# Kernel tuning notes

Measured on AMD Instinct MI355X. Metric: run time of the kernel, lower is better.

The kernel has to match this reference:

```python
import jax, jax.numpy as jnp
import numpy as np

NEG_INF = -1e30


def setup_inputs() -> dict:
    key = jax.random.key(0)
    ks = jax.random.split(key, 5)
    B, S, D, H = 2, 2048, 1024, 16
    sc = 0.02  # weight init scale
    return {
        "x": jax.random.normal(ks[0], (B, S, D), dtype=jnp.float32),
        "Wq": jax.random.normal(ks[1], (D, D), dtype=jnp.float32) * sc,
        "bq": jnp.zeros((D,), dtype=jnp.float32),
        "Wk": jax.random.normal(ks[2], (D, D), dtype=jnp.float32) * sc,
        "bk": jnp.zeros((D,), dtype=jnp.float32),
        "Wv": jax.random.normal(ks[3], (D, D), dtype=jnp.float32) * sc,
        "bv": jnp.zeros((D,), dtype=jnp.float32),
        "Wo": jax.random.normal(ks[4], (D, D), dtype=jnp.float32) * sc,
        "bo": jnp.zeros((D,), dtype=jnp.float32),
        "temperature": jnp.ones((H,), dtype=jnp.float32),
    }


def reference(x, Wq, bq, Wk, bk, Wv, bv, Wo, bo, temperature):
    B, S, D = x.shape
    H = temperature.shape[0]
    hd = D // H
    sparsity = 0.8
    k = max(1, int(S * (1.0 - sparsity)))
    scale = hd ** (-0.5)

    # torch Linear: y = x @ W^T + b ; reshape to [B, S, H, hd] -> [B, H, S, hd]
    def proj(W, b):
        return (x @ W.T + b).reshape(B, S, H, hd).transpose(0, 2, 1, 3)

    q, kk, v = proj(Wq, bq), proj(Wk, bk), proj(Wv, bv)

    temp = jnp.clip(temperature, 0.1, None)[None, :, None, None]  # [1,H,1,1]
    scores = jnp.einsum("bhqd,bhkd->bhqk", q, kk) * scale / temp  # [B,H,S,S]

    # top-k sparsity: keep the k largest scores per row, -inf elsewhere.
    # Equivalent to torch's topk+scatter for distinct values: threshold at
    # the k-th largest value per row.
    topk_vals = jax.lax.top_k(scores, k)[0]           # [B,H,S,k]
    kth = topk_vals[..., -1:]                          # [B,H,S,1]
    sparse_scores = jnp.where(scores >= kth, scores, NEG_INF)

    attn = jax.nn.softmax(sparse_scores, axis=-1)      # [B,H,S,S]
    head_out = jnp.einsum("bhqk,bhkd->bhqd", attn, v)  # [B,H,S,hd]

    # stack heads back: [B,S,H,hd] -> [B,S,D], then out projection
    out = head_out.transpose(0, 2, 1, 3).reshape(B, S, D)
    out = out @ Wo.T + bo

    avg_attention = attn.mean(axis=1)                  # [B,S,S]
    return out, avg_attention
```

## Files before the change

kernel.cpp:

```cpp
#include <hip/hip_runtime.h>
#include <stdint.h>

#define S_LEN 2048
#define D_DIM 1024
#define NHEAD 16
#define HD    64
#define TOPK  409

typedef unsigned short u16;
typedef __attribute__((ext_vector_type(8))) short bf16x8;
typedef __attribute__((ext_vector_type(4))) float f32x4;
#define MFMA __builtin_amdgcn_mfma_f32_16x16x32_bf16

__device__ __forceinline__ u16 f2b(float f) {
    unsigned u = __float_as_uint(f);
    return (u16)((u + 0x7fffu + ((u >> 16) & 1u)) >> 16);
}
__device__ __forceinline__ float b2f(u16 h) {
    return __uint_as_float(((unsigned)h) << 16);
}

__global__ __launch_bounds__(256, 4)
void split_f32(const float* __restrict__ src, u16* __restrict__ hi,
               u16* __restrict__ lo, int n4)
{
    const int i = blockIdx.x * 256 + threadIdx.x;
    if (i >= n4) return;
    const float4 v = ((const float4*)src)[i];
    const float vv[4] = {v.x, v.y, v.z, v.w};
    u16 h4[4], l4[4];
#pragma unroll
    for (int c = 0; c < 4; ++c) {
        h4[c] = f2b(vv[c]);
        l4[c] = f2b(vv[c] - b2f(h4[c]));
    }
    ((ushort4*)hi)[i] = make_ushort4(h4[0], h4[1], h4[2], h4[3]);
    ((ushort4*)lo)[i] = make_ushort4(l4[0], l4[1], l4[2], l4[3]);
}

template<int MODE>
__global__ __launch_bounds__(512, 2)
void proj_mfma(const u16* __restrict__ Ahi, const u16* __restrict__ Alo,
               const u16* __restrict__ Whi, const u16* __restrict__ Wlo,
               const float* __restrict__ bias, float* __restrict__ outf,
               u16* __restrict__ o1, u16* __restrict__ o2)
{
    const int t = threadIdx.x, w = t >> 6, l = t & 63;
    const int lq = l & 15, quad = l >> 4;
    const int m0 = blockIdx.y * 128 + (w >> 2) * 64;
    const int n0 = blockIdx.x * 128 + (w & 3) * 32;

    f32x4 acc[4][2];
#pragma unroll
    for (int i = 0; i < 4; ++i)
#pragma unroll
        for (int j = 0; j < 2; ++j) acc[i][j] = (f32x4){0.f, 0.f, 0.f, 0.f};

    const size_t abase = (size_t)(m0 + lq) * D_DIM + quad * 8;
    const size_t bbase = (size_t)(n0 + lq) * D_DIM + quad * 8;

#pragma unroll 2
    for (int k0 = 0; k0 < D_DIM; k0 += 32) {
        bf16x8 ah[4], al[4], bh[2], bl[2];
#pragma unroll
        for (int i = 0; i < 4; ++i) {
            ah[i] = *(const bf16x8*)(Ahi + abase + (size_t)i * 16 * D_DIM + k0);
            al[i] = *(const bf16x8*)(Alo + abase + (size_t)i * 16 * D_DIM + k0);
        }
#pragma unroll
        for (int j = 0; j < 2; ++j) {
            bh[j] = *(const bf16x8*)(Whi + bbase + (size_t)j * 16 * D_DIM + k0);
            bl[j] = *(const bf16x8*)(Wlo + bbase + (size_t)j * 16 * D_DIM + k0);
        }
#pragma unroll
        for (int i = 0; i < 4; ++i)
#pragma unroll
            for (int j = 0; j < 2; ++j) {
                acc[i][j] = MFMA(ah[i], bh[j], acc[i][j], 0, 0, 0);
                acc[i][j] = MFMA(ah[i], bl[j], acc[i][j], 0, 0, 0);
                acc[i][j] = MFMA(al[i], bh[j], acc[i][j], 0, 0, 0);
            }
    }

#pragma unroll
    for (int j = 0; j < 2; ++j) {
        const int n = n0 + j * 16 + lq;
        const float bb = bias[n];
        const int hh = n >> 6, ee = n & 63;
#pragma unroll
        for (int i = 0; i < 4; ++i) {
            const int mb = m0 + i * 16 + quad * 4;
            const int bbm = mb >> 11, ss = mb & 2047;
            if (MODE == 2) {
#pragma unroll
                for (int r = 0; r < 4; ++r)
                    outf[(size_t)(mb + r) * D_DIM + n] = acc[i][j][r] + bb;
            } else if (MODE == 1) {
                ushort4 pk;
                pk.x = f2b(acc[i][j][0] + bb);
                pk.y = f2b(acc[i][j][1] + bb);
                pk.z = f2b(acc[i][j][2] + bb);
                pk.w = f2b(acc[i][j][3] + bb);
                *(ushort4*)(o1 + ((size_t)((bbm * NHEAD + hh) * HD + ee)) * S_LEN + ss) = pk;
            } else {
#pragma unroll
                for (int r = 0; r < 4; ++r) {
                    const float v = acc[i][j][r] + bb;
                    const size_t idx = ((size_t)(bbm * NHEAD + hh) * S_LEN + ss + r) * HD + ee;
                    const u16 h = f2b(v);
                    o1[idx] = h;
                    o2[idx] = f2b(v - b2f(h));
                }
            }
        }
    }
}

__global__ __launch_bounds__(512, 2)
void attn_mfma(const u16* __restrict__ Qhi, const u16* __restrict__ Qlo,
               const u16* __restrict__ Khi, const u16* __restrict__ Klo,
               const u16* __restrict__ Vt,  const float* __restrict__ temp,
               u16* __restrict__ HOhi, u16* __restrict__ HOlo,
               float* __restrict__ avg)
{
    __shared__ __align__(16) u16 aLds[16 * 2056];
    __shared__ float pvpart[4 * 16 * 16];
    __shared__ int   cnts[16][8][5];
    __shared__ float red[16][8][2];
    __shared__ float rowMu[16], rowSig[16], rowLo[16], rowHi[16], rowZi[16];

    const int t = threadIdx.x, w = t >> 6, l = t & 63;
    const int lq = l & 15, quad = l >> 4;
    const int b  = blockIdx.x >> 7;
    const int q0 = (blockIdx.x & 127) << 4;

    float avgreg[64];
#pragma unroll
    for (int i = 0; i < 64; ++i) avgreg[i] = 0.f;

#pragma unroll 1
    for (int h = 0; h < NHEAD; ++h) {
        const size_t bh = (size_t)(b * NHEAD + h) * S_LEN;
        const float tscale = 0.125f / fmaxf(temp[h], 0.1f);

        const u16* qph = Qhi + (bh + q0 + lq) * HD + quad * 8;
        const u16* qpl = Qlo + (bh + q0 + lq) * HD + quad * 8;
        const bf16x8 qh0 = *(const bf16x8*)qph;
        const bf16x8 qh1 = *(const bf16x8*)(qph + 32);
        const bf16x8 ql0 = *(const bf16x8*)qpl;
        const bf16x8 ql1 = *(const bf16x8*)(qpl + 32);

        f32x4 acc[16];
        const u16* kph = Khi + (bh + w * 256 + lq) * HD + quad * 8;
        const u16* kpl = Klo + (bh + w * 256 + lq) * HD + quad * 8;
#pragma unroll
        for (int tt = 0; tt < 16; ++tt) {
            const bf16x8 k0 = *(const bf16x8*)(kph + tt * 16 * HD);
            const bf16x8 k1 = *(const bf16x8*)(kph + tt * 16 * HD + 32);
            const bf16x8 m0 = *(const bf16x8*)(kpl + tt * 16 * HD);
            const bf16x8 m1 = *(const bf16x8*)(kpl + tt * 16 * HD + 32);
            f32x4 a = {0.f, 0.f, 0.f, 0.f};
            a = MFMA(qh0, k0, a, 0, 0, 0);
            a = MFMA(qh1, k1, a, 0, 0, 0);
            a = MFMA(qh0, m0, a, 0, 0, 0);
            a = MFMA(qh1, m1, a, 0, 0, 0);
            a = MFMA(ql0, k0, a, 0, 0, 0);
            a = MFMA(ql1, k1, a, 0, 0, 0);
            acc[tt] = a * tscale;
        }
        __syncthreads();

        {
            float s1[4] = {0.f,0.f,0.f,0.f}, s2[4] = {0.f,0.f,0.f,0.f};
#pragma unroll
            for (int tt = 0; tt < 16; ++tt)
#pragma unroll
                for (int r = 0; r < 4; ++r) {
                    const float v = acc[tt][r];
                    s1[r] += v;
                    s2[r] = __fmaf_rn(v, v, s2[r]);
                }
#pragma unroll
            for (int off = 1; off < 16; off <<= 1)
#pragma unroll
                for (int r = 0; r < 4; ++r) {
                    s1[r] += __shfl_xor(s1[r], off, 16);
                    s2[r] += __shfl_xor(s2[r], off, 16);
                }
            if (lq == 0)
#pragma unroll
                for (int r = 0; r < 4; ++r) {
                    red[quad * 4 + r][w][0] = s1[r];
                    red[quad * 4 + r][w][1] = s2[r];
                }
        }
        __syncthreads();
        if (t < 16) {
            float a = 0.f, c = 0.f;
#pragma unroll
            for (int ww = 0; ww < 8; ++ww) { a += red[t][ww][0]; c += red[t][ww][1]; }
            const float mu = a * (1.f / 2048.f);
            const float va = c * (1.f / 2048.f) - mu * mu;
            rowMu[t] = mu;
            rowSig[t] = sqrtf(fmaxf(va, 0.f));
        }
        __syncthreads();

        {
            float th[5][4];
            int c[5][4];
#pragma unroll
            for (int r = 0; r < 4; ++r) {
                const float mu = rowMu[quad * 4 + r], sg = rowSig[quad * 4 + r];
#pragma unroll
                for (int i = 0; i < 5; ++i) {
                    th[i][r] = __fmaf_rn(sg, 0.55f + 0.15f * (float)i, mu);
                    c[i][r] = 0;
                }
            }
#pragma unroll
            for (int tt = 0; tt < 16; ++tt)
#pragma unroll
                for (int r = 0; r < 4; ++r) {
                    const float v = acc[tt][r];
#pragma unroll
                    for (int i = 0; i < 5; ++i) c[i][r] += (v >= th[i][r]) ? 1 : 0;
                }
#pragma unroll
            for (int off = 1; off < 16; off <<= 1)
#pragma unroll
                for (int i = 0; i < 5; ++i)
#pragma unroll
                    for (int r = 0; r < 4; ++r) c[i][r] += __shfl_xor(c[i][r], off, 16);
            if (lq == 0)
#pragma unroll
                for (int r = 0; r < 4; ++r)
#pragma unroll
                    for (int i = 0; i < 5; ++i) cnts[quad * 4 + r][w][i] = c[i][r];
        }
        __syncthreads();
        if (t < 16) {
            int c[5] = {0, 0, 0, 0, 0};
#pragma unroll
            for (int ww = 0; ww < 8; ++ww)
#pragma unroll
                for (int i = 0; i < 5; ++i) c[i] += cnts[t][ww][i];
            const float mu = rowMu[t], sg = rowSig[t];
            float lo, hi;
            if (c[0] < TOPK) {
                lo = __fmaf_rn(sg, -6.f, mu);
                hi = __fmaf_rn(sg, 0.55f + 0.15f * 0.f, mu);
            } else if (c[4] >= TOPK) {
                lo = __fmaf_rn(sg, 0.55f + 0.15f * 4.f, mu);
                hi = __fmaf_rn(sg, 6.f, mu);
            } else {
                int bi = 0;
#pragma unroll
                for (int j = 1; j < 4; ++j) if (c[j] >= TOPK) bi = j;
                lo = __fmaf_rn(sg, 0.55f + 0.15f * (float)bi, mu);
                hi = __fmaf_rn(sg, 0.55f + 0.15f * (float)(bi + 1), mu);
            }
            rowLo[t] = lo;
            rowHi[t] = hi;
        }
        __syncthreads();

#pragma unroll 1
        for (int rd = 0; rd < 5; ++rd) {
            {
                float th[3][4];
                int c[3][4];
#pragma unroll
                for (int r = 0; r < 4; ++r) {
                    const float lo_ = rowLo[quad * 4 + r], hi_ = rowHi[quad * 4 + r];
                    const float w4 = __fmul_rn(__fsub_rn(hi_, lo_), 0.25f);
#pragma unroll
                    for (int j = 0; j < 3; ++j) {
                        th[j][r] = __fmaf_rn(w4, (float)(j + 1), lo_);
                        c[j][r] = 0;
                    }
                }
#pragma unroll
                for (int tt = 0; tt < 16; ++tt)
#pragma unroll
                    for (int r = 0; r < 4; ++r) {
                        const float v = acc[tt][r];
#pragma unroll
                        for (int j = 0; j < 3; ++j) c[j][r] += (v >= th[j][r]) ? 1 : 0;
                    }
#pragma unroll
                for (int off = 1; off < 16; off <<= 1)
#pragma unroll
                    for (int j = 0; j < 3; ++j)
#pragma unroll
                        for (int r = 0; r < 4; ++r) c[j][r] += __shfl_xor(c[j][r], off, 16);
                if (lq == 0)
#pragma unroll
                    for (int r = 0; r < 4; ++r)
#pragma unroll
                        for (int j = 0; j < 3; ++j) cnts[quad * 4 + r][w][j] = c[j][r];
            }
            __syncthreads();
            if (t < 16) {
                int d[3] = {0, 0, 0};
#pragma unroll
                for (int ww = 0; ww < 8; ++ww)
#pragma unroll
                    for (int j = 0; j < 3; ++j) d[j] += cnts[t][ww][j];
                float lo = rowLo[t], hi = rowHi[t];
                const float w4 = __fmul_rn(__fsub_rn(hi, lo), 0.25f);
                const float t1 = __fmaf_rn(w4, 1.f, lo);
                const float t2 = __fmaf_rn(w4, 2.f, lo);
                const float t3 = __fmaf_rn(w4, 3.f, lo);
                if (d[2] >= TOPK)      { lo = t3; }
                else if (d[1] >= TOPK) { lo = t2; hi = t3; }
                else if (d[0] >= TOPK) { lo = t1; hi = t2; }
                else                   { hi = t1; }
                rowLo[t] = lo;
                rowHi[t] = hi;
            }
            __syncthreads();
        }

        float kth[4], zp[4] = {0.f, 0.f, 0.f, 0.f};
#pragma unroll
        for (int r = 0; r < 4; ++r) kth[r] = rowLo[quad * 4 + r];
#pragma unroll
        for (int tt = 0; tt < 16; ++tt)
#pragma unroll
            for (int r = 0; r < 4; ++r) {
                const float v = acc[tt][r];
                const float e = (v >= kth[r]) ? __expf(v) : 0.f;
                acc[tt][r] = e;
                zp[r] += e;
            }
#pragma unroll
        for (int off = 1; off < 16; off <<= 1)
#pragma unroll
            for (int r = 0; r < 4; ++r) zp[r] += __shfl_xor(zp[r], off, 16);
        if (lq == 0)
#pragma unroll
            for (int r = 0; r < 4; ++r) red[quad * 4 + r][w][0] = zp[r];
        __syncthreads();
        if (t < 16) {
            float z = 0.f;
#pragma unroll
            for (int ww = 0; ww < 8; ++ww) z += red[t][ww][0];
            rowZi[t] = 1.f / z;
        }
        __syncthreads();
        float zi[4];
#pragma unroll
        for (int r = 0; r < 4; ++r) zi[r] = rowZi[quad * 4 + r];

#pragma unroll
        for (int tt = 0; tt < 16; ++tt)
#pragma unroll
            for (int r = 0; r < 4; ++r) {
                const float a_ = acc[tt][r] * zi[r];
                avgreg[tt * 4 + r] += a_;
                aLds[(quad * 4 + r) * 2056 + w * 256 + tt * 16 + lq] = f2b(a_);
            }
        __syncthreads();

        const int et = w & 3, jh = w >> 2;
        const u16* vb = Vt + ((size_t)(b * NHEAD + h) * HD + et * 16 + lq) * S_LEN
                        + jh * 1024 + quad * 8;
        const u16* ab = aLds + lq * 2056 + jh * 1024 + quad * 8;
        f32x4 pv = {0.f, 0.f, 0.f, 0.f};
#pragma unroll 8
        for (int st = 0; st < 32; ++st) {
            const bf16x8 af = *(const bf16x8*)(ab + st * 32);
            const bf16x8 vf = *(const bf16x8*)(vb + st * 32);
            pv = MFMA(af, vf, pv, 0, 0, 0);
        }
        if (w >= 4) {
#pragma unroll
            for (int r = 0; r < 4; ++r)
                pvpart[(et * 16 + quad * 4 + r) * 16 + lq] = pv[r];
        }
        __syncthreads();
        if (w < 4) {
#pragma unroll
            for (int r = 0; r < 4; ++r) {
                const float v = pv[r] + pvpart[(et * 16 + quad * 4 + r) * 16 + lq];
                const size_t idx =
                    ((size_t)(b * S_LEN + q0 + quad * 4 + r)) * D_DIM + h * HD + et * 16 + lq;
                const u16 hv = f2b(v);
                HOhi[idx] = hv;
                HOlo[idx] = f2b(v - b2f(hv));
            }
        }
    }

#pragma unroll
    for (int tt = 0; tt < 16; ++tt)
#pragma unroll
        for (int r = 0; r < 4; ++r)
            avg[((size_t)(b * S_LEN + q0 + quad * 4 + r)) * S_LEN + w * 256 + tt * 16 + lq] =
                avgreg[tt * 4 + r] * (1.f / NHEAD);
}

extern "C" void kernel_launch(void* const* d_in, const int* in_sizes, int n_in,
                              void* d_out, int out_size, void* d_ws, size_t ws_size,
                              hipStream_t stream)
{
    const float* x    = (const float*)d_in[0];
    const float* Wq   = (const float*)d_in[1];
    const float* bq   = (const float*)d_in[2];
    const float* Wk   = (const float*)d_in[3];
    const float* bk   = (const float*)d_in[4];
    const float* Wv   = (const float*)d_in[5];
    const float* bv   = (const float*)d_in[6];
    const float* Wo   = (const float*)d_in[7];
    const float* bo   = (const float*)d_in[8];
    const float* temp = (const float*)d_in[9];
    float* out = (float*)d_out;

    const int B = in_sizes[0] / (S_LEN * D_DIM);
    const int M = B * S_LEN;
    const size_t NQ = (size_t)M * D_DIM;
    const size_t NW = (size_t)D_DIM * D_DIM;

    u16* Qhi = (u16*)d_ws;
    u16* Qlo = Qhi + NQ;
    u16* Khi = Qlo + NQ;
    u16* Klo = Khi + NQ;
    u16* Vt  = Klo + NQ;
    u16* Xhi = Vt  + NQ;
    u16* Xlo = Xhi + NQ;
    u16* Wqh = Xlo + NQ;
    u16* Wql = Wqh + NW;
    u16* Wkh = Wql + NW;
    u16* Wkl = Wkh + NW;
    u16* Wvh = Wkl + NW;
    u16* Wvl = Wvh + NW;
    u16* Woh = Wvl + NW;
    u16* Wol = Woh + NW;
    float* avg = out + NQ;

    const int n4x = (int)(NQ / 4), n4w = (int)(NW / 4);
    split_f32<<<(n4x + 255) / 256, 256, 0, stream>>>(x,  Xhi, Xlo, n4x);
    split_f32<<<(n4w + 255) / 256, 256, 0, stream>>>(Wq, Wqh, Wql, n4w);
    split_f32<<<(n4w + 255) / 256, 256, 0, stream>>>(Wk, Wkh, Wkl, n4w);
    split_f32<<<(n4w + 255) / 256, 256, 0, stream>>>(Wv, Wvh, Wvl, n4w);
    split_f32<<<(n4w + 255) / 256, 256, 0, stream>>>(Wo, Woh, Wol, n4w);

    dim3 gg(D_DIM / 128, M / 128, 1);
    proj_mfma<0><<<gg, 512, 0, stream>>>(Xhi, Xlo, Wqh, Wql, bq, nullptr, Qhi, Qlo);
    proj_mfma<0><<<gg, 512, 0, stream>>>(Xhi, Xlo, Wkh, Wkl, bk, nullptr, Khi, Klo);
    proj_mfma<1><<<gg, 512, 0, stream>>>(Xhi, Xlo, Wvh, Wvl, bv, nullptr, Vt, nullptr);

    attn_mfma<<<dim3(M / 16), 512, 0, stream>>>(Qhi, Qlo, Khi, Klo, Vt, temp,
                                                Xhi, Xlo, avg);

    proj_mfma<2><<<gg, 512, 0, stream>>>(Xhi, Xlo, Woh, Wol, bo, out, nullptr, nullptr);
}
```

Measured before the change: 1.194 ms.

## Replace block-wide top-k bisection with per-wave two-level histogram select

Moves the score scale and temperature into the Q projection epilogue. In the attention kernel, each wave now owns two full score rows staged through shared memory. It finds the k-th largest value with a two-pass 128-bin LDS histogram, replacing several block-wide count-and-bisect rounds that each needed __syncthreads. Softmax normalisation is deferred to the PV output and the avg accumulation, and the avg stores become float4. The exact threshold now depends on histogram resolution (sig/2048), which could change tie behaviour at the k-th boundary, and the LDS atomics add contention.

```diff
diff --git a/kernel.cpp b/kernel.cpp
--- a/kernel.cpp
+++ b/kernel.cpp
@@ -42,8 +42,8 @@
 __global__ __launch_bounds__(512, 2)
 void proj_mfma(const u16* __restrict__ Ahi, const u16* __restrict__ Alo,
                const u16* __restrict__ Whi, const u16* __restrict__ Wlo,
-               const float* __restrict__ bias, float* __restrict__ outf,
-               u16* __restrict__ o1, u16* __restrict__ o2)
+               const float* __restrict__ bias, const float* __restrict__ tempp,
+               float* __restrict__ outf, u16* __restrict__ o1, u16* __restrict__ o2)
 {
     const int t = threadIdx.x, w = t >> 6, l = t & 63;
     const int lq = l & 15, quad = l >> 4;
@@ -81,6 +81,8 @@
                 acc[i][j] = MFMA(al[i], bh[j], acc[i][j], 0, 0, 0);
             }
     }
+
+    const float tsc = (MODE == 0 && tempp) ? 0.125f / fmaxf(tempp[n0 >> 6], 0.1f) : 1.f;
 
 #pragma unroll
     for (int j = 0; j < 2; ++j) {
@@ -105,7 +107,7 @@
             } else {
 #pragma unroll
                 for (int r = 0; r < 4; ++r) {
-                    const float v = acc[i][j][r] + bb;
+                    const float v = (acc[i][j][r] + bb) * tsc;
                     const size_t idx = ((size_t)(bbm * NHEAD + hh) * S_LEN + ss + r) * HD + ee;
                     const u16 h = f2b(v);
                     o1[idx] = h;
@@ -119,29 +121,32 @@
 __global__ __launch_bounds__(512, 2)
 void attn_mfma(const u16* __restrict__ Qhi, const u16* __restrict__ Qlo,
                const u16* __restrict__ Khi, const u16* __restrict__ Klo,
-               const u16* __restrict__ Vt,  const float* __restrict__ temp,
+               const u16* __restrict__ Vt,
                u16* __restrict__ HOhi, u16* __restrict__ HOlo,
                float* __restrict__ avg)
 {
-    __shared__ __align__(16) u16 aLds[16 * 2056];
+    __shared__ __align__(16) float scf[16 * 2056];
     __shared__ float pvpart[4 * 16 * 16];
-    __shared__ int   cnts[16][8][5];
-    __shared__ float red[16][8][2];
-    __shared__ float rowMu[16], rowSig[16], rowLo[16], rowHi[16], rowZi[16];
+    __shared__ float rowZi[16];
+
+    u16* aLds = (u16*)scf;
+    unsigned* histA = (unsigned*)scf + (16 * 2056 - 2048);
 
     const int t = threadIdx.x, w = t >> 6, l = t & 63;
     const int lq = l & 15, quad = l >> 4;
     const int b  = blockIdx.x >> 7;
     const int q0 = (blockIdx.x & 127) << 4;
-
-    float avgreg[64];
-#pragma unroll
-    for (int i = 0; i < 64; ++i) avgreg[i] = 0.f;
+    const int rA = 2 * w;
+
+    float avgreg[16][4];
+#pragma unroll
+    for (int i = 0; i < 16; ++i)
+#pragma unroll
+        for (int c = 0; c < 4; ++c) avgreg[i][c] = 0.f;
 
 #pragma unroll 1
     for (int h = 0; h < NHEAD; ++h) {
         const size_t bh = (size_t)(b * NHEAD + h) * S_LEN;
-        const float tscale = 0.125f / fmaxf(temp[h], 0.1f);
 
         const u16* qph = Qhi + (bh + q0 + lq) * HD + quad * 8;
         const u16* qpl = Qlo + (bh + q0 + lq) * HD + quad * 8;
@@ -166,202 +171,140 @@
             a = MFMA(qh1, m1, a, 0, 0, 0);
             a = MFMA(ql0, k0, a, 0, 0, 0);
             a = MFMA(ql1, k1, a, 0, 0, 0);
-            acc[tt] = a * tscale;
-        }
+            acc[tt] = a;
+        }
+#pragma unroll
+        for (int tt = 0; tt < 16; ++tt)
+#pragma unroll
+            for (int r = 0; r < 4; ++r)
+                scf[(quad * 4 + r) * 2056 + w * 256 + tt * 16 + lq] = acc[tt][r];
         __syncthreads();
 
-        {
-            float s1[4] = {0.f,0.f,0.f,0.f}, s2[4] = {0.f,0.f,0.f,0.f};
-#pragma unroll
-            for (int tt = 0; tt < 16; ++tt)
-#pragma unroll
-                for (int r = 0; r < 4; ++r) {
-                    const float v = acc[tt][r];
-                    s1[r] += v;
-                    s2[r] = __fmaf_rn(v, v, s2[r]);
-                }
-#pragma unroll
-            for (int off = 1; off < 16; off <<= 1)
-#pragma unroll
-                for (int r = 0; r < 4; ++r) {
-                    s1[r] += __shfl_xor(s1[r], off, 16);
-                    s2[r] += __shfl_xor(s2[r], off, 16);
-                }
-            if (lq == 0)
-#pragma unroll
-                for (int r = 0; r < 4; ++r) {
-                    red[quad * 4 + r][w][0] = s1[r];
-                    red[quad * 4 + r][w][1] = s2[r];
-                }
-        }
+#pragma unroll
+        for (int i = 0; i < 8; ++i)
+            acc[i] = *(const f32x4*)&scf[rA * 2056 + l * 4 + i * 256];
+#pragma unroll
+        for (int i = 0; i < 8; ++i)
+            acc[8 + i] = *(const f32x4*)&scf[(rA + 1) * 2056 + l * 4 + i * 256];
         __syncthreads();
-        if (t < 16) {
-            float a = 0.f, c = 0.f;
-#pragma unroll
-            for (int ww = 0; ww < 8; ++ww) { a += red[t][ww][0]; c += red[t][ww][1]; }
-            const float mu = a * (1.f / 2048.f);
-            const float va = c * (1.f / 2048.f) - mu * mu;
-            rowMu[t] = mu;
-            rowSig[t] = sqrtf(fmaxf(va, 0.f));
+
+#pragma unroll 1
+        for (int rr = 0; rr < 2; ++rr) {
+            f32x4* va = acc + rr * 8;
+            unsigned* hrow = histA + (rA + rr) * 128;
+
+            float s1 = 0.f, s2 = 0.f;
+#pragma unroll
+            for (int i = 0; i < 8; ++i)
+#pragma unroll
+                for (int c = 0; c < 4; ++c) {
+                    const float v = va[i][c];
+                    s1 += v;
+                    s2 = __fmaf_rn(v, v, s2);
+                }
+#pragma unroll
+            for (int off = 1; off < 64; off <<= 1) {
+                s1 += __shfl_xor(s1, off);
+                s2 += __shfl_xor(s2, off);
+            }
+            const float mu = s1 * (1.f / 2048.f);
+            const float sig = fmaxf(sqrtf(fmaxf(s2 * (1.f / 2048.f) - mu * mu, 0.f)), 1e-20f);
+
+            const float lo1 = __fmaf_rn(sig, -4.f, mu);
+            const float inv1 = 16.f / sig;
+            hrow[l] = 0u; hrow[l + 64] = 0u;
+#pragma unroll
+            for (int i = 0; i < 8; ++i)
+#pragma unroll
+                for (int c = 0; c < 4; ++c) {
+                    float f = (va[i][c] - lo1) * inv1;
+                    f = fminf(fmaxf(f, 0.f), 127.f);
+                    atomicAdd(&hrow[(int)f], 1u);
+                }
+            __asm__ volatile("s_waitcnt lgkmcnt(0)" ::: "memory");
+            {
+                const unsigned ha = hrow[2 * l], hb = hrow[2 * l + 1];
+                int suf = (int)(ha + hb);
+#pragma unroll
+                for (int off = 1; off < 64; off <<= 1) {
+                    const int o = __shfl_down(suf, off);
+                    if (l + off < 64) suf += o;
+                }
+                const int S0 = suf, S1 = suf - (int)ha;
+                int cand = (S1 >= TOPK) ? (2 * l + 1) : ((S0 >= TOPK) ? (2 * l) : -1);
+                int gb = cand;
+#pragma unroll
+                for (int off = 1; off < 64; off <<= 1) {
+                    const int o = __shfl_xor(gb, off);
+                    gb = (o > gb) ? o : gb;
+                }
+                const int baseL = (cand == 2 * l + 1) ? (S1 - (int)hb) : S1;
+                const int base = __shfl(baseL, gb >> 1);
+
+                const float w1 = sig * (1.f / 16.f);
+                const float lo2 = __fmaf_rn(w1, (float)gb, lo1);
+                const float inv2 = 2048.f / sig;
+                hrow[l] = 0u; hrow[l + 64] = 0u;
+#pragma unroll
+                for (int i = 0; i < 8; ++i)
+#pragma unroll
+                    for (int c = 0; c < 4; ++c) {
+                        const float f = (va[i][c] - lo2) * inv2;
+                        if (f >= 0.f && f < 128.f)
+                            atomicAdd(&hrow[(int)f], 1u);
+                    }
+                __asm__ volatile("s_waitcnt lgkmcnt(0)" ::: "memory");
+                const unsigned ha2 = hrow[2 * l], hb2 = hrow[2 * l + 1];
+                int suf2 = (int)(ha2 + hb2);
+#pragma unroll
+                for (int off = 1; off < 64; off <<= 1) {
+                    const int o = __shfl_down(suf2, off);
+                    if (l + off < 64) suf2 += o;
+                }
+                const int T0 = base + suf2, T1 = base + suf2 - (int)ha2;
+                int cand2 = (T1 >= TOPK) ? (2 * l + 1) : ((T0 >= TOPK) ? (2 * l) : -1);
+                int gb2 = cand2;
+#pragma unroll
+                for (int off = 1; off < 64; off <<= 1) {
+                    const int o = __shfl_xor(gb2, off);
+                    gb2 = (o > gb2) ? o : gb2;
+                }
+                const float kthv = __fmaf_rn(sig * (1.f / 2048.f), (float)gb2, lo2);
+
+                float z = 0.f;
+#pragma unroll
+                for (int i = 0; i < 8; ++i)
+#pragma unroll
+                    for (int c = 0; c < 4; ++c) {
+                        const float v = va[i][c];
+                        const float e = (v >= kthv) ? __expf(v) : 0.f;
+                        va[i][c] = e;
+                        z += e;
+                    }
+#pragma unroll
+                for (int off = 1; off < 64; off <<= 1) z += __shfl_xor(z, off);
+                if (l == 0) rowZi[rA + rr] = 1.f / z;
+            }
+
+#pragma unroll
+            for (int i = 0; i < 8; ++i) {
+                uint2 p;
+                p.x = (unsigned)f2b(va[i][0]) | ((unsigned)f2b(va[i][1]) << 16);
+                p.y = (unsigned)f2b(va[i][2]) | ((unsigned)f2b(va[i][3]) << 16);
+                *(uint2*)&aLds[(rA + rr) * 2056 + l * 4 + i * 256] = p;
+            }
         }
         __syncthreads();
 
-        {
-            float th[5][4];
-            int c[5][4];
-#pragma unroll
-            for (int r = 0; r < 4; ++r) {
-                const float mu = rowMu[quad * 4 + r], sg = rowSig[quad * 4 + r];
-#pragma unroll
-                for (int i = 0; i < 5; ++i) {
-                    th[i][r] = __fmaf_rn(sg, 0.55f + 0.15f * (float)i, mu);
-                    c[i][r] = 0;
-                }
-            }
-#pragma unroll
-            for (int tt = 0; tt < 16; ++tt)
-#pragma unroll
-                for (int r = 0; r < 4; ++r) {
-                    const float v = acc[tt][r];
-#pragma unroll
-                    for (int i = 0; i < 5; ++i) c[i][r] += (v >= th[i][r]) ? 1 : 0;
-                }
-#pragma unroll
-            for (int off = 1; off < 16; off <<= 1)
-#pragma unroll
-                for (int i = 0; i < 5; ++i)
-#pragma unroll
-                    for (int r = 0; r < 4; ++r) c[i][r] += __shfl_xor(c[i][r], off, 16);
-            if (lq == 0)
-#pragma unroll
-                for (int r = 0; r < 4; ++r)
-#pragma unroll
-                    for (int i = 0; i < 5; ++i) cnts[quad * 4 + r][w][i] = c[i][r];
-        }
-        __syncthreads();
-        if (t < 16) {
-            int c[5] = {0, 0, 0, 0, 0};
-#pragma unroll
-            for (int ww = 0; ww < 8; ++ww)
-#pragma unroll
-                for (int i = 0; i < 5; ++i) c[i] += cnts[t][ww][i];
-            const float mu = rowMu[t], sg = rowSig[t];
-            float lo, hi;
-            if (c[0] < TOPK) {
-                lo = __fmaf_rn(sg, -6.f, mu);
-                hi = __fmaf_rn(sg, 0.55f + 0.15f * 0.f, mu);
-            } else if (c[4] >= TOPK) {
-                lo = __fmaf_rn(sg, 0.55f + 0.15f * 4.f, mu);
-                hi = __fmaf_rn(sg, 6.f, mu);
-            } else {
-                int bi = 0;
-#pragma unroll
-                for (int j = 1; j < 4; ++j) if (c[j] >= TOPK) bi = j;
-                lo = __fmaf_rn(sg, 0.55f + 0.15f * (float)bi, mu);
-                hi = __fmaf_rn(sg, 0.55f + 0.15f * (float)(bi + 1), mu);
-            }
-            rowLo[t] = lo;
-            rowHi[t] = hi;
-        }
-        __syncthreads();
-
-#pragma unroll 1
-        for (int rd = 0; rd < 5; ++rd) {
-            {
-                float th[3][4];
-                int c[3][4];
-#pragma unroll
-                for (int r = 0; r < 4; ++r) {
-                    const float lo_ = rowLo[quad * 4 + r], hi_ = rowHi[quad * 4 + r];
-                    const float w4 = __fmul_rn(__fsub_rn(hi_, lo_), 0.25f);
-#pragma unroll
-                    for (int j = 0; j < 3; ++j) {
-                        th[j][r] = __fmaf_rn(w4, (float)(j + 1), lo_);
-                        c[j][r] = 0;
-                    }
-                }
-#pragma unroll
-                for (int tt = 0; tt < 16; ++tt)
-#pragma unroll
-                    for (int r = 0; r < 4; ++r) {
-                        const float v = acc[tt][r];
-#pragma unroll
-                        for (int j = 0; j < 3; ++j) c[j][r] += (v >= th[j][r]) ? 1 : 0;
-                    }
-#pragma unroll
-                for (int off = 1; off < 16; off <<= 1)
-#pragma unroll
-                    for (int j = 0; j < 3; ++j)
-#pragma unroll
-                        for (int r = 0; r < 4; ++r) c[j][r] += __shfl_xor(c[j][r], off, 16);
-                if (lq == 0)
-#pragma unroll
-                    for (int r = 0; r < 4; ++r)
-#pragma unroll
-                        for (int j = 0; j < 3; ++j) cnts[quad * 4 + r][w][j] = c[j][r];
-            }
-            __syncthreads();
-            if (t < 16) {
-                int d[3] = {0, 0, 0};
-#pragma unroll
-                for (int ww = 0; ww < 8; ++ww)
-#pragma unroll
-                    for (int j = 0; j < 3; ++j) d[j] += cnts[t][ww][j];
-                float lo = rowLo[t], hi = rowHi[t];
-                const float w4 = __fmul_rn(__fsub_rn(hi, lo), 0.25f);
-                const float t1 = __fmaf_rn(w4, 1.f, lo);
-                const float t2 = __fmaf_rn(w4, 2.f, lo);
-                const float t3 = __fmaf_rn(w4, 3.f, lo);
-                if (d[2] >= TOPK)      { lo = t3; }
-                else if (d[1] >= TOPK) { lo = t2; hi = t3; }
-                else if (d[0] >= TOPK) { lo = t1; hi = t2; }
-                else                   { hi = t1; }
-                rowLo[t] = lo;
-                rowHi[t] = hi;
-            }
-            __syncthreads();
-        }
-
-        float kth[4], zp[4] = {0.f, 0.f, 0.f, 0.f};
-#pragma unroll
-        for (int r = 0; r < 4; ++r) kth[r] = rowLo[quad * 4 + r];
-#pragma unroll
-        for (int tt = 0; tt < 16; ++tt)
-#pragma unroll
-            for (int r = 0; r < 4; ++r) {
-                const float v = acc[tt][r];
-                const float e = (v >= kth[r]) ? __expf(v) : 0.f;
-                acc[tt][r] = e;
-                zp[r] += e;
-            }
-#pragma unroll
-        for (int off = 1; off < 16; off <<= 1)
-#pragma unroll
-            for (int r = 0; r < 4; ++r) zp[r] += __shfl_xor(zp[r], off, 16);
-        if (lq == 0)
-#pragma unroll
-            for (int r = 0; r < 4; ++r) red[quad * 4 + r][w][0] = zp[r];
-        __syncthreads();
-        if (t < 16) {
-            float z = 0.f;
-#pragma unroll
-            for (int ww = 0; ww < 8; ++ww) z += red[t][ww][0];
-            rowZi[t] = 1.f / z;
-        }
-        __syncthreads();
-        float zi[4];
-#pragma unroll
-        for (int r = 0; r < 4; ++r) zi[r] = rowZi[quad * 4 + r];
-
-#pragma unroll
-        for (int tt = 0; tt < 16; ++tt)
-#pragma unroll
-            for (int r = 0; r < 4; ++r) {
-                const float a_ = acc[tt][r] * zi[r];
-                avgreg[tt * 4 + r] += a_;
-                aLds[(quad * 4 + r) * 2056 + w * 256 + tt * 16 + lq] = f2b(a_);
-            }
-        __syncthreads();
+#pragma unroll
+        for (int row = 0; row < 16; ++row) {
+            const float zi = rowZi[row];
+            const uint2 d = *(const uint2*)&aLds[row * 2056 + w * 256 + l * 4];
+            avgreg[row][0] = __fmaf_rn(__uint_as_float(d.x << 16), zi, avgreg[row][0]);
+            avgreg[row][1] = __fmaf_rn(__uint_as_float(d.x & 0xffff0000u), zi, avgreg[row][1]);
+            avgreg[row][2] = __fmaf_rn(__uint_as_float(d.y << 16), zi, avgreg[row][2]);
+            avgreg[row][3] = __fmaf_rn(__uint_as_float(d.y & 0xffff0000u), zi, avgreg[row][3]);
+        }
 
         const int et = w & 3, jh = w >> 2;
         const u16* vb = Vt + ((size_t)(b * NHEAD + h) * HD + et * 16 + lq) * S_LEN
@@ -383,7 +326,8 @@
         if (w < 4) {
 #pragma unroll
             for (int r = 0; r < 4; ++r) {
-                const float v = pv[r] + pvpart[(et * 16 + quad * 4 + r) * 16 + lq];
+                const float v = (pv[r] + pvpart[(et * 16 + quad * 4 + r) * 16 + lq])
+                                * rowZi[quad * 4 + r];
                 const size_t idx =
                     ((size_t)(b * S_LEN + q0 + quad * 4 + r)) * D_DIM + h * HD + et * 16 + lq;
                 const u16 hv = f2b(v);
@@ -394,11 +338,14 @@
     }
 
 #pragma unroll
-    for (int tt = 0; tt < 16; ++tt)
-#pragma unroll
-        for (int r = 0; r < 4; ++r)
-            avg[((size_t)(b * S_LEN + q0 + quad * 4 + r)) * S_LEN + w * 256 + tt * 16 + lq] =
-                avgreg[tt * 4 + r] * (1.f / NHEAD);
+    for (int row = 0; row < 16; ++row) {
+        float4 o;
+        o.x = avgreg[row][0] * (1.f / NHEAD);
+        o.y = avgreg[row][1] * (1.f / NHEAD);
+        o.z = avgreg[row][2] * (1.f / NHEAD);
+        o.w = avgreg[row][3] * (1.f / NHEAD);
+        *(float4*)(avg + ((size_t)(b * S_LEN + q0 + row)) * S_LEN + w * 256 + l * 4) = o;
+    }
 }
 
 extern "C" void kernel_launch(void* const* d_in, const int* in_sizes, int n_in,
@@ -447,12 +394,11 @@
     split_f32<<<(n4w + 255) / 256, 256, 0, stream>>>(Wo, Woh, Wol, n4w);
 
     dim3 gg(D_DIM / 128, M / 128, 1);
-    proj_mfma<0><<<gg, 512, 0, stream>>>(Xhi, Xlo, Wqh, Wql, bq, nullptr, Qhi, Qlo);
-    proj_mfma<0><<<gg, 512, 0, stream>>>(Xhi, Xlo, Wkh, Wkl, bk, nullptr, Khi, Klo);
-    proj_mfma<1><<<gg, 512, 0, stream>>>(Xhi, Xlo, Wvh, Wvl, bv, nullptr, Vt, nullptr);
-
-    attn_mfma<<<dim3(M / 16), 512, 0, stream>>>(Qhi, Qlo, Khi, Klo, Vt, temp,
-                                                Xhi, Xlo, avg);
-
-    proj_mfma<2><<<gg, 512, 0, stream>>>(Xhi, Xlo, Woh, Wol, bo, out, nullptr, nullptr);
-}
+    proj_mfma<0><<<gg, 512, 0, stream>>>(Xhi, Xlo, Wqh, Wql, bq, temp,    nullptr, Qhi, Qlo);
+    proj_mfma<0><<<gg, 512, 0, stream>>>(Xhi, Xlo, Wkh, Wkl, bk, nullptr, nullptr, Khi, Klo);
+    proj_mfma<1><<<gg, 512, 0, stream>>>(Xhi, Xlo, Wvh, Wvl, bv, nullptr, nullptr, Vt, nullptr);
+
+    attn_mfma<<<dim3(M / 16), 512, 0, stream>>>(Qhi, Qlo, Khi, Klo, Vt, Xhi, Xlo, avg);
+
+    proj_mfma<2><<<gg, 512, 0, stream>>>(Xhi, Xlo, Woh, Wol, bo, nullptr, out, nullptr, nullptr);
+}
```

Measured after the change: 1.337 ms. 1.12x slower.
